# Kernel tuning notes

Measured on AMD Instinct MI355X. Metric: run time of the kernel, lower is better.

## Reference

```python
import jax, jax.numpy as jnp
import numpy as np

NUM_EMB = 10_000_000
EMB_DIM = 3
B = 16384
HIST = 50
K = 128


def setup_inputs() -> dict:
    key = jax.random.key(0)
    k1, k2, k3, k4, k5, k6, k7, k8, k9 = jax.random.split(key, 9)
    eb_input = jax.random.randint(k1, (B * HIST,), 0, NUM_EMB, dtype=jnp.int64)
    eb_offset = (jnp.arange(B, dtype=jnp.int64) * HIST)  # bag starts
    mlp_input = jax.random.normal(k2, (B, K), dtype=jnp.float32)
    # learned params
    emb_weight = jax.random.normal(k3, (NUM_EMB, EMB_DIM), dtype=jnp.float32)
    w0 = jax.random.normal(k4, (12, K), dtype=jnp.float32) * (1.0 / np.sqrt(K))
    b0 = jax.random.normal(k5, (12,), dtype=jnp.float32) * 0.01
    w1 = jax.random.normal(k6, (6, 12), dtype=jnp.float32) * (1.0 / np.sqrt(12))
    b1 = jax.random.normal(k7, (6,), dtype=jnp.float32) * 0.01
    w2 = jax.random.normal(k8, (3, 6), dtype=jnp.float32) * (1.0 / np.sqrt(6))
    b2 = jax.random.normal(k9, (3,), dtype=jnp.float32) * 0.01
    return {"eb_input": eb_input, "eb_offset": eb_offset, "mlp_input": mlp_input,
            "emb_weight": emb_weight, "w0": w0, "b0": b0, "w1": w1, "b1": b1,
            "w2": w2, "b2": b2}


def _embedding_bag_mean(weight, indices, offsets, num_bags):
    # bag id for each index position (offsets are sorted bag starts, offsets[0]=0)
    n = indices.shape[0]
    seg = jnp.searchsorted(offsets, jnp.arange(n, dtype=offsets.dtype), side='right') - 1
    rows = weight[indices]                                   # [N, 3] gather
    sums = jax.ops.segment_sum(rows, seg, num_segments=num_bags)          # [B, 3]
    cnts = jax.ops.segment_sum(jnp.ones((n,), weight.dtype), seg, num_segments=num_bags)
    return sums / jnp.maximum(cnts, 1.0)[:, None]            # mean mode; empty bag -> 0


def reference(eb_input, eb_offset, mlp_input, emb_weight, w0, b0, w1, b1, w2, b2):
    # All 3 EmbeddingBags alias the SAME module (python list * 3), so one lookup suffices.
    eb_out = _embedding_bag_mean(emb_weight, eb_input, eb_offset, mlp_input.shape[0])
    h = mlp_input @ w0.T + b0
    h = h @ w1.T + b1
    mlp_out = h @ w2.T + b2                                   # [B, 3]
    return jnp.concatenate([eb_out, eb_out, eb_out, mlp_out], axis=1)  # [B, 12]
```

## Files before the change

### kernel.cpp

```cpp
#include <hip/hip_runtime.h>


#define KDIM 128

struct F3 { float x, y, z; };

__global__ __launch_bounds__(256) void fused_embbag_mlp_kernel(
    const int* __restrict__ eb_input,
    const int* __restrict__ eb_offset,
    const float* __restrict__ mlp_input,
    const float* __restrict__ emb_weight,
    const float* __restrict__ w0,
    const float* __restrict__ b0,
    const float* __restrict__ w1,
    const float* __restrict__ b1,
    const float* __restrict__ w2,
    const float* __restrict__ b2,
    float* __restrict__ out,
    int n_indices, int num_bags)
{
    __shared__ float wsT[KDIM * 4];
    __shared__ float bc[4];

    const int tid = threadIdx.x;
    if (tid < KDIM) {
        float t[6];
        #pragma unroll
        for (int i = 0; i < 6; ++i) {
            float acc = 0.f;
            #pragma unroll
            for (int j = 0; j < 12; ++j)
                acc += w1[i * 12 + j] * w0[j * KDIM + tid];
            t[i] = acc;
        }
        #pragma unroll
        for (int o = 0; o < 3; ++o) {
            float acc = 0.f;
            #pragma unroll
            for (int i = 0; i < 6; ++i)
                acc += w2[o * 6 + i] * t[i];
            wsT[tid * 4 + o] = acc;
        }
        wsT[tid * 4 + 3] = 0.f;
        if (tid == 0) {
            float tb[6];
            #pragma unroll
            for (int i = 0; i < 6; ++i) {
                float acc = 0.f;
                #pragma unroll
                for (int j = 0; j < 12; ++j)
                    acc += w1[i * 12 + j] * b0[j];
                tb[i] = acc + b1[i];
            }
            #pragma unroll
            for (int o = 0; o < 3; ++o) {
                float acc = 0.f;
                #pragma unroll
                for (int i = 0; i < 6; ++i)
                    acc += w2[o * 6 + i] * tb[i];
                bc[o] = acc + b2[o];
            }
            bc[3] = 0.f;
        }
    }
    __syncthreads();

    const int lane = tid & 63;
    const int wave = tid >> 6;
    const int bag  = blockIdx.x * (blockDim.x >> 6) + wave;
    if (bag >= num_bags) return;

    const int start = eb_offset[bag];
    const int end   = (bag + 1 < num_bags) ? eb_offset[bag + 1] : n_indices;
    const int cnt   = end - start;

    const float2 x  = *(const float2*)(mlp_input + bag * KDIM + lane * 2);
    const float4 t0 = *(const float4*)(wsT + lane * 8);
    const float4 t1 = *(const float4*)(wsT + lane * 8 + 4);
    float m0 = x.x * t0.x + x.y * t1.x;
    float m1 = x.x * t0.y + x.y * t1.y;
    float m2 = x.x * t0.z + x.y * t1.z;

    float sx = 0.f, sy = 0.f, sz = 0.f;
    if (lane < cnt) {
        const int idx = eb_input[start + lane];
        const F3 r = *(const F3*)(emb_weight + idx * 3);
        sx = r.x; sy = r.y; sz = r.z;
        for (int p = start + lane + 64; p < end; p += 64) {
            const int i2 = eb_input[p];
            const F3 r2 = *(const F3*)(emb_weight + i2 * 3);
            sx += r2.x; sy += r2.y; sz += r2.z;
        }
    }

    #pragma unroll
    for (int off = 1; off <= 32; off <<= 1) {
        sx += __shfl_xor(sx, off, 64);
        sy += __shfl_xor(sy, off, 64);
        sz += __shfl_xor(sz, off, 64);
        m0 += __shfl_xor(m0, off, 64);
        m1 += __shfl_xor(m1, off, 64);
        m2 += __shfl_xor(m2, off, 64);
    }

    if (lane < 12) {
        float v;
        if (lane < 9) {
            const float inv = 1.0f / fmaxf((float)cnt, 1.0f);
            const int cc = lane % 3;
            v = (cc == 0 ? sx : (cc == 1 ? sy : sz)) * inv;
        } else {
            const int cc = lane - 9;
            v = (cc == 0 ? m0 : (cc == 1 ? m1 : m2)) + bc[cc];
        }
        out[bag * 12 + lane] = v;
    }
}

extern "C" void kernel_launch(void* const* d_in, const int* in_sizes, int n_in,
                              void* d_out, int out_size, void* d_ws, size_t ws_size,
                              hipStream_t stream) {
    const int*   eb_input   = (const int*)d_in[0];
    const int*   eb_offset  = (const int*)d_in[1];
    const float* mlp_input  = (const float*)d_in[2];
    const float* emb_weight = (const float*)d_in[3];
    const float* w0 = (const float*)d_in[4];
    const float* b0 = (const float*)d_in[5];
    const float* w1 = (const float*)d_in[6];
    const float* b1 = (const float*)d_in[7];
    const float* w2 = (const float*)d_in[8];
    const float* b2 = (const float*)d_in[9];
    float* out = (float*)d_out;
    (void)d_ws; (void)ws_size;

    const int n_indices = in_sizes[0];
    const int num_bags  = in_sizes[1];

    const int waves_per_block = 4;
    const int grid = (num_bags + waves_per_block - 1) / waves_per_block;
    fused_embbag_mlp_kernel<<<grid, 256, 0, stream>>>(
        eb_input, eb_offset, mlp_input, emb_weight,
        w0, b0, w1, b1, w2, b2, out, n_indices, num_bags);
}
```

Measured before the change: 196.3 us.

## Bucket lookups by embedding row range before gathering, accumulate bags with atomics

Replaces the one-wave-per-bag gather with a four-kernel pipeline. A scatter pass bins (index, bag) pairs into buckets keyed by embedding row range. A gather pass reads the embedding rows bucket by bucket and adds them into per-bag sums with float atomics. A finalize pass computes the mean and the folded MLP. The aim is more local reads of the 120MB table, at the cost of extra launches, millions of global atomics, pair traffic through workspace and a spill path for overfull buckets.

```diff
diff --git a/kernel.cpp b/kernel.cpp
--- a/kernel.cpp
+++ b/kernel.cpp
@@ -2,26 +2,174 @@
 
 
 #define KDIM 128
+#define NB   16384
+#define CAP  128
 
 struct F3 { float x, y, z; };
 
-__global__ __launch_bounds__(256) void fused_embbag_mlp_kernel(
-    const int* __restrict__ eb_input,
+__global__ __launch_bounds__(256) void zero_kernel(
+    unsigned int* __restrict__ counts, unsigned int* __restrict__ spill_cnt,
+    float* __restrict__ tmp, int ntmp) {
+    const int i = blockIdx.x * blockDim.x + threadIdx.x;
+    if (i < NB) counts[i] = 0u;
+    if (i < ntmp) tmp[i] = 0.f;
+    if (i == 0) spill_cnt[0] = 0u;
+}
+
+__global__ __launch_bounds__(256) void scatter_kernel(
+    const int* __restrict__ eb_input, const int* __restrict__ eb_offset,
+    unsigned int* __restrict__ counts, unsigned int* __restrict__ spill_cnt,
+    unsigned long long* __restrict__ pairs, unsigned long long* __restrict__ spill,
+    int n, int num_bags) {
+    const int p = blockIdx.x * blockDim.x + threadIdx.x;
+    if (p >= n) return;
+    const unsigned int idx = (unsigned)eb_input[p];
+    int lo = 0, hi = num_bags - 1;
+    while (lo < hi) {
+        const int mid = (lo + hi + 1) >> 1;
+        if (eb_offset[mid] <= p) lo = mid; else hi = mid - 1;
+    }
+    const unsigned long long pk = ((unsigned long long)idx << 32) | (unsigned)lo;
+    const unsigned int b = idx >> 10;
+    const unsigned int c = atomicAdd(&counts[b], 1u);
+    if (c < CAP) {
+        pairs[(size_t)b * CAP + c] = pk;
+    } else {
+        const unsigned int sc = atomicAdd(spill_cnt, 1u);
+        spill[sc] = pk;
+    }
+}
+
+__global__ __launch_bounds__(256) void gather_kernel(
+    const unsigned long long* __restrict__ pairs,
+    const unsigned long long* __restrict__ spill,
+    const unsigned int* __restrict__ counts,
+    const unsigned int* __restrict__ spill_cnt,
+    const float* __restrict__ emb_weight,
+    float* __restrict__ tmp, int n) {
+    const long long i = (long long)blockIdx.x * blockDim.x + threadIdx.x;
+    unsigned long long pk;
+    if (i < (long long)NB * CAP) {
+        const unsigned int b = (unsigned int)(i >> 7);
+        const unsigned int j = (unsigned int)(i & (CAP - 1));
+        const unsigned int cb = counts[b];
+        if (j >= (cb < CAP ? cb : CAP)) return;
+        pk = pairs[i];
+    } else {
+        const long long k = i - (long long)NB * CAP;
+        if (k >= (long long)spill_cnt[0]) return;
+        pk = spill[k];
+    }
+    const unsigned int idx = (unsigned int)(pk >> 32);
+    const unsigned int bag = (unsigned int)(pk & 0xffffffffu);
+    const F3 r = *(const F3*)(emb_weight + (size_t)idx * 3);
+    atomicAdd(&tmp[bag * 3 + 0], r.x);
+    atomicAdd(&tmp[bag * 3 + 1], r.y);
+    atomicAdd(&tmp[bag * 3 + 2], r.z);
+}
+
+__global__ __launch_bounds__(256) void finalize_kernel(
     const int* __restrict__ eb_offset,
     const float* __restrict__ mlp_input,
-    const float* __restrict__ emb_weight,
-    const float* __restrict__ w0,
-    const float* __restrict__ b0,
-    const float* __restrict__ w1,
-    const float* __restrict__ b1,
-    const float* __restrict__ w2,
-    const float* __restrict__ b2,
+    const float* __restrict__ tmp,
+    const float* __restrict__ w0, const float* __restrict__ b0,
+    const float* __restrict__ w1, const float* __restrict__ b1,
+    const float* __restrict__ w2, const float* __restrict__ b2,
     float* __restrict__ out,
     int n_indices, int num_bags)
 {
     __shared__ float wsT[KDIM * 4];
     __shared__ float bc[4];
 
+    const int tid = threadIdx.x;
+    if (tid < KDIM) {
+        float t[6];
+        #pragma unroll
+        for (int i = 0; i < 6; ++i) {
+            float acc = 0.f;
+            #pragma unroll
+            for (int j = 0; j < 12; ++j)
+                acc += w1[i * 12 + j] * w0[j * KDIM + tid];
+            t[i] = acc;
+        }
+        #pragma unroll
+        for (int o = 0; o < 3; ++o) {
+            float acc = 0.f;
+            #pragma unroll
+            for (int i = 0; i < 6; ++i)
+                acc += w2[o * 6 + i] * t[i];
+            wsT[tid * 4 + o] = acc;
+        }
+        wsT[tid * 4 + 3] = 0.f;
+        if (tid == 0) {
+            float tb[6];
+            #pragma unroll
+            for (int i = 0; i < 6; ++i) {
+                float acc = 0.f;
+                #pragma unroll
+                for (int j = 0; j < 12; ++j)
+                    acc += w1[i * 12 + j] * b0[j];
+                tb[i] = acc + b1[i];
+            }
+            #pragma unroll
+            for (int o = 0; o < 3; ++o) {
+                float acc = 0.f;
+                #pragma unroll
+                for (int i = 0; i < 6; ++i)
+                    acc += w2[o * 6 + i] * tb[i];
+                bc[o] = acc + b2[o];
+            }
+            bc[3] = 0.f;
+        }
+    }
+    __syncthreads();
+
+    const int lane = tid & 63;
+    const int wave = tid >> 6;
+    const int bag  = blockIdx.x * (blockDim.x >> 6) + wave;
+    if (bag >= num_bags) return;
+
+    const int start = eb_offset[bag];
+    const int end   = (bag + 1 < num_bags) ? eb_offset[bag + 1] : n_indices;
+    const int cnt   = end - start;
+
+    const float2 x  = *(const float2*)(mlp_input + bag * KDIM + lane * 2);
+    const float4 t0 = *(const float4*)(wsT + lane * 8);
+    const float4 t1 = *(const float4*)(wsT + lane * 8 + 4);
+    float m0 = x.x * t0.x + x.y * t1.x;
+    float m1 = x.x * t0.y + x.y * t1.y;
+    float m2 = x.x * t0.z + x.y * t1.z;
+
+    #pragma unroll
+    for (int off = 1; off <= 32; off <<= 1) {
+        m0 += __shfl_xor(m0, off, 64);
+        m1 += __shfl_xor(m1, off, 64);
+        m2 += __shfl_xor(m2, off, 64);
+    }
+
+    if (lane < 12) {
+        float v;
+        if (lane < 9) {
+            const float inv = 1.0f / fmaxf((float)cnt, 1.0f);
+            v = tmp[bag * 3 + (lane % 3)] * inv;
+        } else {
+            const int cc = lane - 9;
+            v = (cc == 0 ? m0 : (cc == 1 ? m1 : m2)) + bc[cc];
+        }
+        out[bag * 12 + lane] = v;
+    }
+}
+
+__global__ __launch_bounds__(256) void fused_embbag_mlp_kernel(
+    const int* __restrict__ eb_input, const int* __restrict__ eb_offset,
+    const float* __restrict__ mlp_input, const float* __restrict__ emb_weight,
+    const float* __restrict__ w0, const float* __restrict__ b0,
+    const float* __restrict__ w1, const float* __restrict__ b1,
+    const float* __restrict__ w2, const float* __restrict__ b2,
+    float* __restrict__ out, int n_indices, int num_bags)
+{
+    __shared__ float wsT[KDIM * 4];
+    __shared__ float bc[4];
     const int tid = threadIdx.x;
     if (tid < KDIM) {
         float t[6];
@@ -92,7 +240,6 @@
             sx += r2.x; sy += r2.y; sz += r2.z;
         }
     }
-
     #pragma unroll
     for (int off = 1; off <= 32; off <<= 1) {
         sx += __shfl_xor(sx, off, 64);
@@ -102,13 +249,11 @@
         m1 += __shfl_xor(m1, off, 64);
         m2 += __shfl_xor(m2, off, 64);
     }
-
     if (lane < 12) {
         float v;
         if (lane < 9) {
             const float inv = 1.0f / fmaxf((float)cnt, 1.0f);
-            const int cc = lane % 3;
-            v = (cc == 0 ? sx : (cc == 1 ? sy : sz)) * inv;
+            v = (lane % 3 == 0 ? sx : (lane % 3 == 1 ? sy : sz)) * inv;
         } else {
             const int cc = lane - 9;
             v = (cc == 0 ? m0 : (cc == 1 ? m1 : m2)) + bc[cc];
@@ -131,14 +276,41 @@
     const float* w2 = (const float*)d_in[8];
     const float* b2 = (const float*)d_in[9];
     float* out = (float*)d_out;
-    (void)d_ws; (void)ws_size;
 
     const int n_indices = in_sizes[0];
     const int num_bags  = in_sizes[1];
 
-    const int waves_per_block = 4;
-    const int grid = (num_bags + waves_per_block - 1) / waves_per_block;
-    fused_embbag_mlp_kernel<<<grid, 256, 0, stream>>>(
-        eb_input, eb_offset, mlp_input, emb_weight,
-        w0, b0, w1, b1, w2, b2, out, n_indices, num_bags);
-}
+    const size_t pairs_off = 1ull << 20;
+    const size_t spill_off = pairs_off + (size_t)NB * CAP * 8;
+    const size_t needed    = spill_off + (size_t)n_indices * 8;
+    char* ws = (char*)d_ws;
+
+    if (ws == nullptr || ws_size < needed || n_indices <= 0) {
+        const int grid = (num_bags + 3) / 4;
+        fused_embbag_mlp_kernel<<<grid, 256, 0, stream>>>(
+            eb_input, eb_offset, mlp_input, emb_weight,
+            w0, b0, w1, b1, w2, b2, out, n_indices, num_bags);
+        return;
+    }
+
+    unsigned int* counts    = (unsigned int*)(ws);
+    unsigned int* spill_cnt = (unsigned int*)(ws + 64 * 1024);
+    float*        tmp       = (float*)(ws + 128 * 1024);
+    unsigned long long* pairs = (unsigned long long*)(ws + pairs_off);
+    unsigned long long* spill = (unsigned long long*)(ws + spill_off);
+
+    const int ntmp  = num_bags * 3;
+    const int zmax  = (ntmp > NB) ? ntmp : NB;
+    zero_kernel<<<(zmax + 255) / 256, 256, 0, stream>>>(counts, spill_cnt, tmp, ntmp);
+
+    scatter_kernel<<<(n_indices + 255) / 256, 256, 0, stream>>>(
+        eb_input, eb_offset, counts, spill_cnt, pairs, spill, n_indices, num_bags);
+
+    const long long gtot = (long long)NB * CAP + n_indices;
+    gather_kernel<<<(int)((gtot + 255) / 256), 256, 0, stream>>>(
+        pairs, spill, counts, spill_cnt, emb_weight, tmp, n_indices);
+
+    finalize_kernel<<<(num_bags + 3) / 4, 256, 0, stream>>>(
+        eb_offset, mlp_input, tmp, w0, b0, w1, b1, w2, b2,
+        out, n_indices, num_bags);
+}
```

Measured after the change: 357.9 us. 82.4% more time.
